# Kernel tuning notes

Measured on AMD Instinct MI355X. Metric: run time of the kernel, lower is better.

## Reference

```python
import jax, jax.numpy as jnp
import numpy as np

W_CHAMFER = (1.0, 1.0, 1.0)
W_LAPLACE = 0.5
W_MOVE = 0.1
W_EDGE = 0.1
W_NORMAL = 1.6e-4
W_CONST = 1.0
LAP_CONST = (0.2, 1.0, 1.0)
EPS = 1e-12


def _normalize(x):
    # F.normalize(x, dim=-1): x / max(||x||, eps)
    n = jnp.sqrt(jnp.sum(x * x, axis=-1, keepdims=True))
    return x / jnp.maximum(n, EPS)


def _pairwise_sq(x, y):
    # x: (B,N,3), y: (B,M,3) -> (B,N,M) squared distances, GEMM form
    x2 = jnp.sum(x * x, -1)
    y2 = jnp.sum(y * y, -1)
    xy = jnp.einsum('bnd,bmd->bnm', x, y)
    return x2[:, :, None] + y2[:, None, :] - 2.0 * xy


def _laplace_coord(pts, lap_idx):
    # pts: (B,V,3); lap_idx: (V,10) = [8 neighbor idx (-1 invalid), self, count]
    idx = lap_idx[:, :8]
    mask = idx < 0
    safe = jnp.where(mask, 0, idx)
    nbrs = pts[:, safe]                                  # (B,V,8,3)
    nbrs = jnp.where(mask[None, :, :, None], 0.0, nbrs)
    count = lap_idx[:, -1].astype(pts.dtype)
    return pts - nbrs.sum(2) / count[None, :, None]


def setup_inputs():
    key = jax.random.key(0)
    B, M = 2, 8192
    Vs = (642, 2562, 10242)
    Es = (1920, 7680, 30720)
    ks = jax.random.split(key, 3 + 4 * 3)
    inp = {}
    inp['gt_coord'] = jax.random.normal(ks[0], (B, M, 3), jnp.float32)
    inp['gt_normal'] = _normalize(jax.random.normal(ks[1], (B, M, 3), jnp.float32))
    for i, (V, E) in enumerate(zip(Vs, Es)):
        k0, k1, k2, k3 = ks[3 + 4 * i], ks[4 + 4 * i], ks[5 + 4 * i], ks[6 + 4 * i]
        inp[f'pred_coord_{i}'] = jax.random.normal(k0, (B, V, 3), jnp.float32)
        inp[f'pred_before_{i}'] = inp[f'pred_coord_{i}'] + 0.05 * jax.random.normal(k1, (B, V, 3), jnp.float32)
        inp[f'edges_{i}'] = jax.random.randint(k2, (E, 2), 0, V)
        nbr = jax.random.randint(k3, (V, 8), 0, V)
        nbr = nbr.at[:, 6:].set(-1)                      # 6 valid neighbors, 2 invalid slots
        self_idx = jnp.arange(V)[:, None]
        count = jnp.full((V, 1), 6)
        inp[f'laplace_idx_{i}'] = jnp.concatenate([nbr, self_idx, count], axis=1)
    return inp


def reference(pred_coord_0, pred_coord_1, pred_coord_2, pred_before_0, pred_before_1, pred_before_2, gt_coord, gt_normal, laplace_idx_0, laplace_idx_1, laplace_idx_2, edges_0, edges_1, edges_2):
    preds = (pred_coord_0, pred_coord_1, pred_coord_2)
    befores = (pred_before_0, pred_before_1, pred_before_2)
    laps = (laplace_idx_0, laplace_idx_1, laplace_idx_2)
    edges_all = (edges_0, edges_1, edges_2)
    chamfer_loss = 0.0
    edge_loss = 0.0
    normal_loss = 0.0
    lap_loss = 0.0
    move_loss = 0.0
    for i in range(3):
        pred, before, lap_idx, edges = preds[i], befores[i], laps[i], edges_all[i]
        # shared pairwise distance matrix for chamfer + knn (original recomputes)
        d = _pairwise_sq(pred, gt_coord)                 # (B,V,M)
        chamfer_loss = chamfer_loss + W_CHAMFER[i] * (jnp.mean(jnp.min(d, axis=1)) + jnp.mean(jnp.min(d, axis=2)))
        knn_idx = jnp.argmin(d, axis=2)                  # (B,V): nearest gt per pred pt
        e0, e1 = edges[:, 0], edges[:, 1]
        evec = _normalize(pred[:, e0] - pred[:, e1])     # (B,E,3)
        # faithful to torch: knn.idx.flatten() then index_select -> only batch-0
        # indices ever selected since edge ids < V
        sel = knn_idx.reshape(-1)[e0]
        nrm = _normalize(gt_normal[:, sel])              # (B,E,3)
        normal_loss = normal_loss + jnp.mean(jnp.abs(jnp.sum(evec * nrm, axis=2)))
        edge_loss = edge_loss + 3.0 * jnp.mean((pred[:, e0] - pred[:, e1]) ** 2)
        l1 = _laplace_coord(before, lap_idx)
        l2 = _laplace_coord(pred, lap_idx)
        lap_loss = lap_loss + LAP_CONST[i] * 3.0 * jnp.mean((l1 - l2) ** 2)
        if i > 0:
            move_loss = move_loss + LAP_CONST[i] * 3.0 * jnp.mean((before - pred) ** 2)
    loss = chamfer_loss + W_LAPLACE * lap_loss + W_MOVE * move_loss + W_EDGE * edge_loss + W_NORMAL * normal_loss
    return W_CONST * loss
```

## Files before the change

kernel.cpp:

```cpp
#include <hip/hip_runtime.h>


#define DEV __device__ __forceinline__

typedef __attribute__((ext_vector_type(8))) short bs8;
typedef __attribute__((ext_vector_type(4))) float f32x4;

DEV float blockReduceSum256(float v) {
    #pragma unroll
    for (int o = 32; o > 0; o >>= 1) v += __shfl_down(v, o, 64);
    __shared__ float red4[4];
    int wid = threadIdx.x >> 6;
    if ((threadIdx.x & 63) == 0) red4[wid] = v;
    __syncthreads();
    return (threadIdx.x == 0) ? (red4[0] + red4[1] + red4[2] + red4[3]) : 0.0f;
}

DEV void split3(float u, unsigned short& h, unsigned short& m, unsigned short& l) {
    unsigned a = __float_as_uint(u);
    h = (unsigned short)(a >> 16);
    float r1 = u - __uint_as_float(a & 0xFFFF0000u);
    unsigned bb = __float_as_uint(r1);
    m = (unsigned short)(bb >> 16);
    float r2 = r1 - __uint_as_float(bb & 0xFFFF0000u);
    l = (unsigned short)(__float_as_uint(r2) >> 16);
}

DEV void packGT(const float* __restrict__ gp, char* dst) {
    float x = gp[0], y = gp[1], z = gp[2];
    unsigned short hx,mx,lx, hy,my,ly, hz,mz,lz, nh,nm,nl;
    split3(x,hx,mx,lx); split3(y,hy,my,ly); split3(z,hz,mz,lz);
    float n = fmaf(x,x,fmaf(y,y,z*z));
    split3(n,nh,nm,nl);
    const short ONE = (short)0x3F80;
    bs8 w0 = {(short)hx,(short)hx,(short)mx,(short)hx,(short)lx,(short)mx,(short)hy,(short)hy};
    bs8 w1 = {(short)my,(short)hy,(short)ly,(short)my,(short)hz,(short)hz,(short)mz,(short)hz};
    bs8 w2 = {(short)lz,(short)mz,(short)nh,(short)nm,(short)nl,ONE,ONE,ONE};
    bs8 w3 = {0,0,0,0,0,0,0,0};
    *(bs8*)(dst)       = w0;
    *(bs8*)(dst + 256) = w1;
    *(bs8*)(dst + 512) = w2;
    *(bs8*)(dst + 768) = w3;
}

DEV void packVERT(const float* __restrict__ pp, char* dst) {
    float x = pp[0], y = pp[1], z = pp[2];
    unsigned short hx,mx,lx, hy,my,ly, hz,mz,lz, nh,nm,nl;
    split3(-2.f*x,hx,mx,lx); split3(-2.f*y,hy,my,ly); split3(-2.f*z,hz,mz,lz);
    float n = fmaf(x,x,fmaf(y,y,z*z));
    split3(n,nh,nm,nl);
    const short ONE = (short)0x3F80;
    bs8 w0 = {(short)hx,(short)mx,(short)hx,(short)lx,(short)hx,(short)mx,(short)hy,(short)my};
    bs8 w1 = {(short)hy,(short)ly,(short)hy,(short)my,(short)hz,(short)mz,(short)hz,(short)lz};
    bs8 w2 = {(short)hz,(short)mz,ONE,ONE,ONE,(short)nh,(short)nm,(short)nl};
    bs8 w3 = {0,0,0,0,0,0,0,0};
    *(bs8*)(dst)       = w0;
    *(bs8*)(dst + 256) = w1;
    *(bs8*)(dst + 512) = w2;
    *(bs8*)(dst + 768) = w3;
}

template<bool B0>
DEV void mfmaLoop(const char* SA, const char* SB, char* VML,
                  float (&gmin)[8][4], int embedBase, unsigned embedMask)
{
    const int tid = threadIdx.x;
    const int w = tid >> 6, L = tid & 63, lr = L & 15, lg = L >> 4;
    const char* abase = SA + (w * 8) * 1024 + lg * 256 + lr * 16;
    bs8 af[8];
    #pragma unroll
    for (int g = 0; g < 8; g++) af[g] = *(const bs8*)(abase + g * 1024);
    const f32x4 zero = {0.f, 0.f, 0.f, 0.f};
    const char* bbase = SB + lg * 256 + lr * 16;
    bs8 bf = *(const bs8*)(bbase);
    #pragma unroll 2
    for (int vg = 0; vg < 16; vg++) {
        bs8 bfn = bf;
        if (vg < 15) bfn = *(const bs8*)(bbase + (vg + 1) * 1024);
        float vmin = 3.0e38f;
        int code = embedBase;
        #pragma unroll
        for (int gg = 0; gg < 8; gg++) {
            f32x4 acc = __builtin_amdgcn_mfma_f32_16x16x32_bf16(af[gg], bf, zero, 0, 0, 0);
            gmin[gg][0] = fminf(gmin[gg][0], acc[0]);
            gmin[gg][1] = fminf(gmin[gg][1], acc[1]);
            gmin[gg][2] = fminf(gmin[gg][2], acc[2]);
            gmin[gg][3] = fminf(gmin[gg][3], acc[3]);
            float t = fminf(fminf(fminf(acc[0], acc[1]), acc[2]), acc[3]);
            if (B0) {
                t = fmaxf(t, 0.0f);
                t = __uint_as_float((__float_as_uint(t) & embedMask) | (unsigned)code);
                code += 4;
            }
            vmin = fminf(vmin, t);
        }
        vmin = fminf(vmin, __shfl_xor(vmin, 16));
        vmin = fminf(vmin, __shfl_xor(vmin, 32));
        if (lg == 0) *(float*)(VML + ((vg * 16 + lr) * 4 + w) * 4) = vmin;
        bf = bfn;
    }
}

template<bool STORE>
__global__ __launch_bounds__(256, 3) void kMega2(
    const float* __restrict__ p0, const float* __restrict__ p1, const float* __restrict__ p2,
    const float* __restrict__ b0p, const float* __restrict__ b1p, const float* __restrict__ b2p,
    const int* __restrict__ l0, const int* __restrict__ l1, const int* __restrict__ l2,
    const float* __restrict__ gt, char* ws)
{
    extern __shared__ char smem[];
    int bid = blockIdx.x;
    if (bid == 0 && threadIdx.x == 0) { *(float*)ws = 0.f; *(unsigned*)(ws + 4) = 0u; }
    if (bid < 128) {
        float c = 0.0f;
        int idx = bid * 256 + threadIdx.x;
        if (idx < 26892) {
            int level, V, t;
            const float *pred, *bef; const int* lap;
            if (idx < 1284)      { level = 0; V = 642;   pred = p0; bef = b0p; lap = l0; t = idx; }
            else if (idx < 6408) { level = 1; V = 2562;  pred = p1; bef = b1p; lap = l1; t = idx - 1284; }
            else                 { level = 2; V = 10242; pred = p2; bef = b2p; lap = l2; t = idx - 6408; }
            int b = t / V;
            int v = t - b * V;
            const float* P  = pred + ((size_t)b * V + v) * 3;
            const float* Bf = bef  + ((size_t)b * V + v) * 3;
            float dx = Bf[0] - P[0], dy = Bf[1] - P[1], dz = Bf[2] - P[2];
            float sx = 0.f, sy = 0.f, sz = 0.f;
            const int* Lp = lap + v * 10;
            #pragma unroll
            for (int j = 0; j < 8; j++) {
                int n = Lp[j];
                if (n >= 0) {
                    const float* Pn = pred + ((size_t)b * V + n) * 3;
                    const float* Bn = bef  + ((size_t)b * V + n) * 3;
                    sx += Bn[0] - Pn[0]; sy += Bn[1] - Pn[1]; sz += Bn[2] - Pn[2];
                }
            }
            float invc = 1.0f / (float)Lp[9];
            float lx = dx - sx * invc, ly = dy - sy * invc, lz = dz - sz * invc;
            float sl = fmaf(lx, lx, fmaf(ly, ly, lz * lz));
            float sm = fmaf(dx, dx, fmaf(dy, dy, dz * dz));
            float lapc = (level == 0) ? 0.2f : 1.0f;
            float iBV = 1.0f / (2.0f * (float)V);
            c = sl * (0.5f * lapc * iBV) + ((level > 0) ? sm * (0.1f * lapc * iBV) : 0.0f);
        }
        c = blockReduceSum256(c);
        if (threadIdx.x == 0) ((float*)(ws + 8))[bid] = c;
        return;
    }
    int cid = bid - 128;
    int gtt = cid & 15;
    int t2 = cid >> 4;
    int b = t2 >= 55 ? 1 : 0;
    int vt = t2 - 55 * b;
    int lvl, V, vtl; const float* predL;
    if (vt < 3)       { lvl = 0; V = 642;   vtl = vt;      predL = p0; }
    else if (vt < 14) { lvl = 1; V = 2562;  vtl = vt - 3;  predL = p1; }
    else              { lvl = 2; V = 10242; vtl = vt - 14; predL = p2; }
    char* SA  = smem;
    char* SB  = smem + 32768;
    char* VML = smem + 49152;
    int tid = threadIdx.x;
    {
        int v = vtl * 256 + tid;
        if (v >= V) v -= V;
        packVERT(predL + ((size_t)b * V + v) * 3, SB + (tid >> 4) * 1024 + (tid & 15) * 16);
    }
    #pragma unroll
    for (int k = 0; k < 2; k++) {
        int j = tid + k * 256;
        packGT(gt + ((size_t)b * 8192 + gtt * 512 + j) * 3, SA + (j >> 4) * 1024 + (j & 15) * 16);
    }
    __syncthreads();
    float gmin[8][4];
    #pragma unroll
    for (int g = 0; g < 8; g++) {
        gmin[g][0] = 3.0e38f; gmin[g][1] = 3.0e38f; gmin[g][2] = 3.0e38f; gmin[g][3] = 3.0e38f;
    }
    int w = tid >> 6, L = tid & 63, lg = L >> 4;
    if (b == 0) {
        unsigned mask = STORE ? 0xFFFFFF80u : 0xFFFFF800u;
        int eb = w * 32 + lg + (STORE ? 0 : (gtt << 7));
        mfmaLoop<true>(SA, SB, VML, gmin, eb, mask);
    } else {
        mfmaLoop<false>(SA, SB, VML, gmin, 0, 0u);
    }
    __syncthreads();
    float* GML = (float*)SA;
    #pragma unroll
    for (int gg = 0; gg < 8; gg++) {
        #pragma unroll
        for (int r = 0; r < 4; r++)
            GML[(w * 128 + gg * 16 + lg * 4 + r) * 16 + (L & 15)] = gmin[gg][r];
    }
    __syncthreads();
    {
        float4 vv = *(float4*)(VML + tid * 16);
        float pv = fminf(fminf(vv.x, vv.y), fminf(vv.z, vv.w));
        int padOff = lvl == 0 ? 0 : (lvl == 1 ? 768 : 3584);
        int vs = b * 14080 + padOff + vtl * 256 + tid;
        if (STORE) {
            ((float*)(ws + 54808))[(size_t)gtt * 28160 + vs] = pv;
        } else {
            int v = vtl * 256 + tid;
            if (v < V) atomicMin((unsigned*)(ws + 54808) + vs, __float_as_uint(fmaxf(pv, 0.0f)));
        }
    }
    {
        int tb = lvl == 0 ? 0 : (lvl == 1 ? 3 : 14);
        #pragma unroll
        for (int k = 0; k < 2; k++) {
            int g = tid + k * 256;
            float q = 3.0e38f;
            #pragma unroll
            for (int cc = 0; cc < 16; cc++)
                q = fminf(q, GML[g * 16 + ((cc + tid) & 15)]);
            if (STORE) {
                ((float*)(ws + 1857048))[(size_t)(b * 55 + tb + vtl) * 8192 + gtt * 512 + g] = q;
            } else {
                atomicMin((unsigned*)(ws + 167448) + (((b * 3 + lvl) << 13) + gtt * 512 + g),
                          __float_as_uint(fmaxf(q, 0.0f)));
            }
        }
    }
}

template<bool STORE>
__global__ __launch_bounds__(256) void kCombine2(
    const float* __restrict__ p0, const float* __restrict__ p1, const float* __restrict__ p2,
    const float* __restrict__ gt, char* ws)
{
    int bid = blockIdx.x, tid = threadIdx.x;
    float c = 0.0f;
    if (bid == 302) {
        if (tid < 128) c = ((float*)(ws + 8))[tid];
    } else {
        int idx = bid * 256 + tid;
        if (idx < 28160) {
            int b = idx >= 14080 ? 1 : 0;
            int q = idx - b * 14080;
            int lvl, V, lvlOff, padOff; const float* predL; float inv;
            if (q < 768)       { lvl=0; V=642;   padOff=0;    lvlOff=0;    predL=p0; inv=1.f/1284.f; }
            else if (q < 3584) { lvl=1; V=2562;  padOff=768;  lvlOff=642;  predL=p1; inv=1.f/5124.f; }
            else               { lvl=2; V=10242; padOff=3584; lvlOff=3204; predL=p2; inv=1.f/20484.f; }
            int v = q - padOff;
            if (v < V) {
                float best; int bt = 0; unsigned bits;
                if (STORE) {
                    const float* P = (const float*)(ws + 54808) + idx;
                    best = P[0];
                    #pragma unroll
                    for (int t = 1; t < 16; t++) {
                        float u = P[(size_t)t * 28160];
                        if (u < best) { best = u; bt = t; }
                    }
                    bits = __float_as_uint(best);
                } else {
                    bits = ((const unsigned*)(ws + 54808))[idx];
                    best = __uint_as_float(bits);
                    bt = (bits >> 7) & 15;
                }
                float d;
                if (b == 0) {
                    int code = bits & 0x7F;
                    int m0 = bt * 512 + code * 4;
                    const float* pp = predL + (size_t)v * 3;
                    float px = pp[0], py = pp[1], pz = pp[2];
                    float bd = 3.0e38f; int bm = m0;
                    #pragma unroll
                    for (int u2 = 0; u2 < 4; u2++) {
                        const float* gp = gt + (size_t)(m0 + u2) * 3;
                        float dx = px - gp[0], dy = py - gp[1], dz = pz - gp[2];
                        float dd = fmaf(dx, dx, fmaf(dy, dy, dz * dz));
                        if (dd < bd) { bd = dd; bm = m0 + u2; }
                    }
                    ((int*)(ws + 1024))[lvlOff + v] = bm;
                    d = bd;
                } else {
                    d = best;
                }
                c = d * inv;
            }
        } else if (idx < 77312) {
            int r = idx - 28160;
            int b = r >= 24576 ? 1 : 0;
            int rem = r - b * 24576;
            int lvl = rem >> 13, m = rem & 8191;
            float d;
            if (STORE) {
                int nt = lvl == 0 ? 3 : (lvl == 1 ? 11 : 41);
                int tb = lvl == 0 ? 0 : (lvl == 1 ? 3 : 14);
                const float* P = (const float*)(ws + 1857048) + (size_t)(b * 55 + tb) * 8192 + m;
                d = P[0];
                for (int k2 = 1; k2 < nt; k2++) d = fminf(d, P[(size_t)k2 * 8192]);
            } else {
                d = __uint_as_float(((const unsigned*)(ws + 167448))[((b * 3 + lvl) << 13) + m]);
            }
            c = d * (1.f / 16384.f);
        }
    }
    c = blockReduceSum256(c);
    if (tid == 0) atomicAdd((float*)ws, c);
}

__global__ __launch_bounds__(256) void kEdgeOut(
    const float* __restrict__ p0, const float* __restrict__ p1, const float* __restrict__ p2,
    const int* __restrict__ e0p, const int* __restrict__ e1p, const int* __restrict__ e2p,
    const float* __restrict__ gtn, char* ws, float* __restrict__ out)
{
    const int* knn = (const int*)(ws + 1024);
    int idx = blockIdx.x * 256 + threadIdx.x;
    float c = 0.0f;
    {
        int E, V, lvlOff, t;
        const float* pred; const int* edges;
        if (idx < 3840)       { E = 1920;  V = 642;   lvlOff = 0;    pred = p0; edges = e0p; t = idx; }
        else if (idx < 19200) { E = 7680;  V = 2562;  lvlOff = 642;  pred = p1; edges = e1p; t = idx - 3840; }
        else                  { E = 30720; V = 10242; lvlOff = 3204; pred = p2; edges = e2p; t = idx - 19200; }
        int b = t / E;
        int e = t % E;
        int a0 = edges[e * 2 + 0];
        int a1 = edges[e * 2 + 1];
        const float* P = pred + (size_t)b * V * 3;
        float dx = P[a0 * 3 + 0] - P[a1 * 3 + 0];
        float dy = P[a0 * 3 + 1] - P[a1 * 3 + 1];
        float dz = P[a0 * 3 + 2] - P[a1 * 3 + 2];
        float sq = fmaf(dx, dx, fmaf(dy, dy, dz * dz));
        float inv = 1.0f / fmaxf(sqrtf(sq), 1e-12f);
        int sel = knn[lvlOff + a0];
        const float* nr = gtn + ((size_t)b * 8192 + sel) * 3;
        float nx = nr[0], ny = nr[1], nz = nr[2];
        float invn = 1.0f / fmaxf(sqrtf(fmaf(nx, nx, fmaf(ny, ny, nz * nz))), 1e-12f);
        float dotv = fmaf(dx, nx, fmaf(dy, ny, dz * nz)) * inv * invn;
        float iBE = 1.0f / (2.0f * (float)E);
        c = sq * (0.1f * iBE) + fabsf(dotv) * (0.00016f * iBE);
    }
    c = blockReduceSum256(c);
    if (threadIdx.x == 0) {
        atomicAdd((float*)ws, c);
        __threadfence();
        unsigned t = atomicAdd((unsigned*)(ws + 4), 1u);
        if (t == 314u) out[0] = atomicAdd((float*)ws, 0.0f);
    }
}

extern "C" void kernel_launch(void* const* d_in, const int* in_sizes, int n_in,
                              void* d_out, int out_size, void* d_ws, size_t ws_size,
                              hipStream_t stream) {
    const float *gt, *gtn, *pred[3], *bef[3];
    const int *edg[3], *lapx[3];
    if (in_sizes[0] == 49152) {
        gt  = (const float*)d_in[0];
        gtn = (const float*)d_in[1];
        for (int i = 0; i < 3; i++) {
            pred[i] = (const float*)d_in[2 + 4 * i];
            bef[i]  = (const float*)d_in[3 + 4 * i];
            edg[i]  = (const int*)  d_in[4 + 4 * i];
            lapx[i] = (const int*)  d_in[5 + 4 * i];
        }
    } else {
        for (int i = 0; i < 3; i++) pred[i] = (const float*)d_in[i];
        for (int i = 0; i < 3; i++) bef[i]  = (const float*)d_in[3 + i];
        gt  = (const float*)d_in[6];
        gtn = (const float*)d_in[7];
        for (int i = 0; i < 3; i++) lapx[i] = (const int*)d_in[8 + i];
        for (int i = 0; i < 3; i++) edg[i]  = (const int*)d_in[11 + i];
    }

    char* ws = (char*)d_ws;
    bool store = ws_size >= (size_t)5461528;

    if (store) {
        kMega2<true><<<1888, 256, 53248, stream>>>(pred[0], pred[1], pred[2],
                                                   bef[0], bef[1], bef[2],
                                                   lapx[0], lapx[1], lapx[2], gt, ws);
        kCombine2<true><<<303, 256, 0, stream>>>(pred[0], pred[1], pred[2], gt, ws);
    } else {
        hipMemsetAsync(ws + 54808, 0xFF, 364056 - 54808, stream);
        kMega2<false><<<1888, 256, 53248, stream>>>(pred[0], pred[1], pred[2],
                                                    bef[0], bef[1], bef[2],
                                                    lapx[0], lapx[1], lapx[2], gt, ws);
        kCombine2<false><<<303, 256, 0, stream>>>(pred[0], pred[1], pred[2], gt, ws);
    }
    kEdgeOut<<<315, 256, 0, stream>>>(pred[0], pred[1], pred[2],
                                      edg[0], edg[1], edg[2], gtn, ws, (float*)d_out);
}
```

Baseline: 131.0 us.

## Prepack bf16 split operands once and halve chamfer tile height

Adds a kPack kernel that converts all gt points and padded pred vertices into the bf16 three-way-split MFMA operand layout once in workspace, so the chamfer blocks just copy prepacked tiles into LDS instead of recomputing the split per block. The gt tile per block shrinks from 512 to 256 points, which doubles the grid to 3648 blocks, cuts LDS to 36 KB, and raises launch bounds to 4 blocks per SM. The argmin code embedding, partial-min buffers and combine loop are adjusted for 32 gt tiles, and the GML transpose uses stride 17 to avoid bank conflicts. The cost is an extra kernel launch, a larger workspace requirement, and more partial results to reduce in kCombine2.

```diff
diff --git a/kernel.cpp b/kernel.cpp
--- a/kernel.cpp
+++ b/kernel.cpp
@@ -5,6 +5,15 @@
 
 typedef __attribute__((ext_vector_type(8))) short bs8;
 typedef __attribute__((ext_vector_type(4))) float f32x4;
+
+#define WS_GT   65536
+#define WS_VP   1114112
+#define WS_PA   2916352
+#define WS_PB   6520832
+#define WS_PAu  2916352
+#define WS_PBu  3028992
+
+DEV unsigned long long umin64(unsigned long long a, unsigned long long b) { return a < b ? a : b; }
 
 DEV float blockReduceSum256(float v) {
     #pragma unroll
@@ -60,16 +69,38 @@
     *(bs8*)(dst + 768) = w3;
 }
 
+__global__ __launch_bounds__(256) void kPack(
+    const float* __restrict__ p0, const float* __restrict__ p1, const float* __restrict__ p2,
+    const float* __restrict__ gt, char* ws)
+{
+    int idx = blockIdx.x * 256 + threadIdx.x;
+    if (idx < 16384) {
+        packGT(gt + (size_t)idx * 3, ws + WS_GT + (size_t)(idx >> 4) * 1024 + (idx & 15) * 16);
+    } else if (idx < 44544) {
+        int s = idx - 16384;
+        int b = s >= 14080 ? 1 : 0;
+        int q = s - b * 14080;
+        int V, padOff; const float* predL;
+        if (q < 768)       { V = 642;   padOff = 0;    predL = p0; }
+        else if (q < 3584) { V = 2562;  padOff = 768;  predL = p1; }
+        else               { V = 10242; padOff = 3584; predL = p2; }
+        int u = q - padOff;
+        int v = u - (u >= V ? V : 0);
+        packVERT(predL + ((size_t)b * V + v) * 3,
+                 ws + WS_VP + (size_t)(s >> 4) * 1024 + (s & 15) * 16);
+    }
+}
+
 template<bool B0>
 DEV void mfmaLoop(const char* SA, const char* SB, char* VML,
-                  float (&gmin)[8][4], int embedBase, unsigned embedMask)
+                  float (&gmin)[4][4], int embedBase, unsigned embedMask)
 {
     const int tid = threadIdx.x;
     const int w = tid >> 6, L = tid & 63, lr = L & 15, lg = L >> 4;
-    const char* abase = SA + (w * 8) * 1024 + lg * 256 + lr * 16;
-    bs8 af[8];
+    const char* abase = SA + (w * 4) * 1024 + lg * 256 + lr * 16;
+    bs8 af[4];
     #pragma unroll
-    for (int g = 0; g < 8; g++) af[g] = *(const bs8*)(abase + g * 1024);
+    for (int g = 0; g < 4; g++) af[g] = *(const bs8*)(abase + g * 1024);
     const f32x4 zero = {0.f, 0.f, 0.f, 0.f};
     const char* bbase = SB + lg * 256 + lr * 16;
     bs8 bf = *(const bs8*)(bbase);
@@ -80,13 +111,13 @@
         float vmin = 3.0e38f;
         int code = embedBase;
         #pragma unroll
-        for (int gg = 0; gg < 8; gg++) {
+        for (int gg = 0; gg < 4; gg++) {
             f32x4 acc = __builtin_amdgcn_mfma_f32_16x16x32_bf16(af[gg], bf, zero, 0, 0, 0);
             gmin[gg][0] = fminf(gmin[gg][0], acc[0]);
             gmin[gg][1] = fminf(gmin[gg][1], acc[1]);
             gmin[gg][2] = fminf(gmin[gg][2], acc[2]);
             gmin[gg][3] = fminf(gmin[gg][3], acc[3]);
-            float t = fminf(fminf(fminf(acc[0], acc[1]), acc[2]), acc[3]);
+            float t = fminf(fminf(acc[0], acc[1]), fminf(acc[2], acc[3]));
             if (B0) {
                 t = fmaxf(t, 0.0f);
                 t = __uint_as_float((__float_as_uint(t) & embedMask) | (unsigned)code);
@@ -102,11 +133,11 @@
 }
 
 template<bool STORE>
-__global__ __launch_bounds__(256, 3) void kMega2(
+__global__ __launch_bounds__(256, 4) void kMega2(
     const float* __restrict__ p0, const float* __restrict__ p1, const float* __restrict__ p2,
     const float* __restrict__ b0p, const float* __restrict__ b1p, const float* __restrict__ b2p,
     const int* __restrict__ l0, const int* __restrict__ l1, const int* __restrict__ l2,
-    const float* __restrict__ gt, char* ws)
+    char* ws)
 {
     extern __shared__ char smem[];
     int bid = blockIdx.x;
@@ -149,78 +180,71 @@
         return;
     }
     int cid = bid - 128;
-    int gtt = cid & 15;
-    int t2 = cid >> 4;
+    int gtt = cid & 31;
+    int t2 = cid >> 5;
     int b = t2 >= 55 ? 1 : 0;
     int vt = t2 - 55 * b;
-    int lvl, V, vtl; const float* predL;
-    if (vt < 3)       { lvl = 0; V = 642;   vtl = vt;      predL = p0; }
-    else if (vt < 14) { lvl = 1; V = 2562;  vtl = vt - 3;  predL = p1; }
-    else              { lvl = 2; V = 10242; vtl = vt - 14; predL = p2; }
+    int lvl, vtl, V, padOff, tb;
+    if (vt < 3)       { lvl = 0; vtl = vt;      V = 642;   padOff = 0;    tb = 0; }
+    else if (vt < 14) { lvl = 1; vtl = vt - 3;  V = 2562;  padOff = 768;  tb = 3; }
+    else              { lvl = 2; vtl = vt - 14; V = 10242; padOff = 3584; tb = 14; }
     char* SA  = smem;
-    char* SB  = smem + 32768;
-    char* VML = smem + 49152;
+    char* SB  = smem + 16384;
+    char* VML = smem + 32768;
     int tid = threadIdx.x;
     {
-        int v = vtl * 256 + tid;
-        if (v >= V) v -= V;
-        packVERT(predL + ((size_t)b * V + v) * 3, SB + (tid >> 4) * 1024 + (tid & 15) * 16);
-    }
+        const char* gsrc = ws + WS_GT + ((size_t)b * 8192 + gtt * 256) * 64;
+        const char* vsrc = ws + WS_VP + ((size_t)(b * 14080 + padOff + vtl * 256)) * 64;
+        #pragma unroll
+        for (int j = 0; j < 4; j++) {
+            *(bs8*)(SA + j * 4096 + tid * 16) = *(const bs8*)(gsrc + j * 4096 + (size_t)tid * 16);
+            *(bs8*)(SB + j * 4096 + tid * 16) = *(const bs8*)(vsrc + j * 4096 + (size_t)tid * 16);
+        }
+    }
+    __syncthreads();
+    float gmin[4][4];
     #pragma unroll
-    for (int k = 0; k < 2; k++) {
-        int j = tid + k * 256;
-        packGT(gt + ((size_t)b * 8192 + gtt * 512 + j) * 3, SA + (j >> 4) * 1024 + (j & 15) * 16);
-    }
-    __syncthreads();
-    float gmin[8][4];
-    #pragma unroll
-    for (int g = 0; g < 8; g++) {
+    for (int g = 0; g < 4; g++) {
         gmin[g][0] = 3.0e38f; gmin[g][1] = 3.0e38f; gmin[g][2] = 3.0e38f; gmin[g][3] = 3.0e38f;
     }
     int w = tid >> 6, L = tid & 63, lg = L >> 4;
     if (b == 0) {
-        unsigned mask = STORE ? 0xFFFFFF80u : 0xFFFFF800u;
-        int eb = w * 32 + lg + (STORE ? 0 : (gtt << 7));
+        unsigned mask = STORE ? 0xFFFFFFC0u : 0xFFFFF800u;
+        int eb = w * 16 + lg + (STORE ? 0 : (gtt << 6));
         mfmaLoop<true>(SA, SB, VML, gmin, eb, mask);
     } else {
         mfmaLoop<false>(SA, SB, VML, gmin, 0, 0u);
     }
     __syncthreads();
-    float* GML = (float*)SA;
+    float* GML = (float*)smem;
     #pragma unroll
-    for (int gg = 0; gg < 8; gg++) {
+    for (int gg = 0; gg < 4; gg++) {
         #pragma unroll
         for (int r = 0; r < 4; r++)
-            GML[(w * 128 + gg * 16 + lg * 4 + r) * 16 + (L & 15)] = gmin[gg][r];
+            GML[(w * 64 + gg * 16 + lg * 4 + r) * 17 + (L & 15)] = gmin[gg][r];
     }
     __syncthreads();
     {
         float4 vv = *(float4*)(VML + tid * 16);
         float pv = fminf(fminf(vv.x, vv.y), fminf(vv.z, vv.w));
-        int padOff = lvl == 0 ? 0 : (lvl == 1 ? 768 : 3584);
         int vs = b * 14080 + padOff + vtl * 256 + tid;
         if (STORE) {
-            ((float*)(ws + 54808))[(size_t)gtt * 28160 + vs] = pv;
+            ((float*)(ws + WS_PA))[(size_t)gtt * 28160 + vs] = pv;
         } else {
-            int v = vtl * 256 + tid;
-            if (v < V) atomicMin((unsigned*)(ws + 54808) + vs, __float_as_uint(fmaxf(pv, 0.0f)));
+            if (vtl * 256 + tid < V)
+                atomicMin((unsigned*)(ws + WS_PAu) + vs, __float_as_uint(fmaxf(pv, 0.0f)));
         }
     }
     {
-        int tb = lvl == 0 ? 0 : (lvl == 1 ? 3 : 14);
+        float q = 3.0e38f;
         #pragma unroll
-        for (int k = 0; k < 2; k++) {
-            int g = tid + k * 256;
-            float q = 3.0e38f;
-            #pragma unroll
-            for (int cc = 0; cc < 16; cc++)
-                q = fminf(q, GML[g * 16 + ((cc + tid) & 15)]);
-            if (STORE) {
-                ((float*)(ws + 1857048))[(size_t)(b * 55 + tb + vtl) * 8192 + gtt * 512 + g] = q;
-            } else {
-                atomicMin((unsigned*)(ws + 167448) + (((b * 3 + lvl) << 13) + gtt * 512 + g),
-                          __float_as_uint(fmaxf(q, 0.0f)));
-            }
+        for (int cc = 0; cc < 16; cc++)
+            q = fminf(q, GML[tid * 17 + ((cc + tid) & 15)]);
+        if (STORE) {
+            ((float*)(ws + WS_PB))[(size_t)(b * 55 + tb + vtl) * 8192 + gtt * 256 + tid] = q;
+        } else {
+            atomicMin((unsigned*)(ws + WS_PBu) + (((b * 3 + lvl) << 13) + gtt * 256 + tid),
+                      __float_as_uint(fmaxf(q, 0.0f)));
         }
     }
 }
@@ -247,23 +271,23 @@
             if (v < V) {
                 float best; int bt = 0; unsigned bits;
                 if (STORE) {
-                    const float* P = (const float*)(ws + 54808) + idx;
+                    const float* P = (const float*)(ws + WS_PA) + idx;
                     best = P[0];
-                    #pragma unroll
-                    for (int t = 1; t < 16; t++) {
+                    #pragma unroll 8
+                    for (int t = 1; t < 32; t++) {
                         float u = P[(size_t)t * 28160];
                         if (u < best) { best = u; bt = t; }
                     }
                     bits = __float_as_uint(best);
                 } else {
-                    bits = ((const unsigned*)(ws + 54808))[idx];
+                    bits = ((const unsigned*)(ws + WS_PAu))[idx];
                     best = __uint_as_float(bits);
-                    bt = (bits >> 7) & 15;
+                    bt = (bits >> 6) & 31;
                 }
                 float d;
                 if (b == 0) {
-                    int code = bits & 0x7F;
-                    int m0 = bt * 512 + code * 4;
+                    int code = bits & 0x3F;
+                    int m0 = bt * 256 + code * 4;
                     const float* pp = predL + (size_t)v * 3;
                     float px = pp[0], py = pp[1], pz = pp[2];
                     float bd = 3.0e38f; int bm = m0;
@@ -290,11 +314,11 @@
             if (STORE) {
                 int nt = lvl == 0 ? 3 : (lvl == 1 ? 11 : 41);
                 int tb = lvl == 0 ? 0 : (lvl == 1 ? 3 : 14);
-                const float* P = (const float*)(ws + 1857048) + (size_t)(b * 55 + tb) * 8192 + m;
+                const float* P = (const float*)(ws + WS_PB) + (size_t)(b * 55 + tb) * 8192 + m;
                 d = P[0];
                 for (int k2 = 1; k2 < nt; k2++) d = fminf(d, P[(size_t)k2 * 8192]);
             } else {
-                d = __uint_as_float(((const unsigned*)(ws + 167448))[((b * 3 + lvl) << 13) + m]);
+                d = __uint_as_float(((const unsigned*)(ws + WS_PBu))[((b * 3 + lvl) << 13) + m]);
             }
             c = d * (1.f / 16384.f);
         }
@@ -368,18 +392,19 @@
     }
 
     char* ws = (char*)d_ws;
-    bool store = ws_size >= (size_t)5461528;
-
+    bool store = ws_size >= (size_t)10125312;
+
+    kPack<<<174, 256, 0, stream>>>(pred[0], pred[1], pred[2], gt, ws);
     if (store) {
-        kMega2<true><<<1888, 256, 53248, stream>>>(pred[0], pred[1], pred[2],
+        kMega2<true><<<3648, 256, 36864, stream>>>(pred[0], pred[1], pred[2],
                                                    bef[0], bef[1], bef[2],
-                                                   lapx[0], lapx[1], lapx[2], gt, ws);
+                                                   lapx[0], lapx[1], lapx[2], ws);
         kCombine2<true><<<303, 256, 0, stream>>>(pred[0], pred[1], pred[2], gt, ws);
     } else {
-        hipMemsetAsync(ws + 54808, 0xFF, 364056 - 54808, stream);
-        kMega2<false><<<1888, 256, 53248, stream>>>(pred[0], pred[1], pred[2],
+        hipMemsetAsync(ws + WS_PAu, 0xFF, 3225600 - WS_PAu, stream);
+        kMega2<false><<<3648, 256, 36864, stream>>>(pred[0], pred[1], pred[2],
                                                     bef[0], bef[1], bef[2],
-                                                    lapx[0], lapx[1], lapx[2], gt, ws);
+                                                    lapx[0], lapx[1], lapx[2], ws);
         kCombine2<false><<<303, 256, 0, stream>>>(pred[0], pred[1], pred[2], gt, ws);
     }
     kEdgeOut<<<315, 256, 0, stream>>>(pred[0], pred[1], pred[2],
```

Result: slower. 134.5 us (+2.7%).
